# Kernel optimization log

Hardware: AMD Instinct MI355X
Metric: run time of the kernel (lower is better)

Reference implementation:

```python
import jax, jax.numpy as jnp
import numpy as np

B, T, C, H, N_LAYER, LAYER_ID = 4, 2048, 1024, 16, 12, 6
N = C // H
Q = 256  # T % 256 == 0 -> chunk size used by the module


def setup_inputs():
    key = jax.random.key(0)
    ks = jax.random.split(key, 9)
    r0 = LAYER_ID / (N_LAYER - 1)
    r1 = 1.0 - LAYER_ID / N_LAYER
    ddd = (jnp.arange(C, dtype=jnp.float32) / C)[None, None, :]
    h = jnp.arange(C, dtype=jnp.float32)
    s = 1.0 / np.sqrt(C)
    return {
        "x": jax.random.normal(ks[0], (B, T, C), jnp.float32),
        "time_maa_x": 1.0 - ddd ** r1,
        "time_maa_w": 1.0 - ddd ** r1,
        "time_maa_k": 1.0 - ddd ** r1,
        "time_maa_v": 1.0 - (ddd ** r1 + 0.3 * r0),
        "time_maa_r": 1.0 - ddd ** (0.5 * r1),
        "maa_w1": jax.random.uniform(ks[1], (C, 4 * 32), jnp.float32, minval=-0.01, maxval=0.01),
        "maa_w2": jax.random.uniform(ks[2], (4, 32, C), jnp.float32, minval=-0.01, maxval=0.01),
        "decay_w1": jax.random.uniform(ks[3], (C, 64), jnp.float32, minval=-0.01, maxval=0.01),
        "decay_w2": jax.random.uniform(ks[4], (64, C), jnp.float32, minval=-0.01, maxval=0.01),
        "time_decay": (-6.0 + 5.0 * (h / (C - 1)) ** (0.7 + 1.3 * r0))[None, None, :],
        "time_faaaa": (r0 * (1.0 - h / (C - 1))).reshape(1, H, 1, 1, N),
        "Wr": jax.random.normal(ks[5], (C, C), jnp.float32) * s,
        "Wk": jax.random.normal(ks[6], (C, C), jnp.float32) * s,
        "Wv": jax.random.normal(ks[7], (C, C), jnp.float32) * s,
        "Wo": jax.random.normal(ks[8], (C, C), jnp.float32) * s,
        "ln_g": jnp.ones((C,), jnp.float32),
        "ln_b": jnp.zeros((C,), jnp.float32),
    }


def _forward(x, time_maa_x, time_maa_w, time_maa_k, time_maa_v, time_maa_r,
             maa_w1, maa_w2, decay_w1, decay_w2, time_decay, time_faaaa,
             Wr, Wk, Wv, Wo, ln_g, ln_b):
    b, t, c = x.shape
    nc = t // Q
    # time_shift: zero-pad one step at front of time axis, drop last step
    xx = jnp.pad(x, ((0, 0), (1, 0), (0, 0)))[:, :-1] - x
    xxx = x + xx * time_maa_x
    m = jnp.tanh(xxx @ maa_w1).reshape(b, t, 4, -1)  # [B,T,4,32]
    m = jnp.einsum('btfd,fdc->fbtc', m, maa_w2)       # [4,B,T,C]
    mw, mk, mv, mr = m[0], m[1], m[2], m[3]
    xw = x + xx * (time_maa_w + mw)
    xk = x + xx * (time_maa_k + mk)
    xv = x + xx * (time_maa_v + mv)
    xr = x + xx * (time_maa_r + mr)
    r = (xr @ Wr).reshape(b, t, H, N).transpose(0, 2, 1, 3)  # [B,H,T,N]
    k = (xk @ Wk).reshape(b, t, H, N).transpose(0, 2, 1, 3)
    v = (xv @ Wv).reshape(b, t, H, N).transpose(0, 2, 1, 3)
    w = time_decay + jnp.tanh(xw @ decay_w1) @ decay_w2      # [B,T,C]
    w = w.reshape(b, t, H, N).transpose(0, 2, 1, 3).mean(axis=-1)  # [B,H,T]
    w_log = -jnp.exp(w)
    wc = w_log.reshape(b, H, nc, Q, 1)
    wc_cum = jnp.cumsum(wc, axis=-2)
    shifted = jnp.pad(wc_cum, ((0, 0), (0, 0), (0, 0), (1, 0), (0, 0)))[..., :-1, :]
    ws_log = wc.sum(axis=-2, keepdims=True)   # [B,H,nc,1,1]
    w_inter = jnp.exp(ws_log - wc_cum)        # [B,H,nc,Q,1]
    w_intra = jnp.exp(wc_cum - wc)            # [B,H,nc,Q,1]
    ws = jnp.exp(ws_log)                      # [B,H,nc,1,1]
    A = shifted - jnp.swapaxes(wc_cum, -1, -2)  # [B,H,nc,Q,Q]
    strict = jnp.tril(jnp.ones((Q, Q), dtype=bool), -1)
    # torch: tril() -> exp() -> tril(-1)  ==  exp on strict-lower, zero elsewhere
    w_mask = jnp.where(strict, jnp.exp(jnp.where(strict, A, 0.0)), 0.0)
    rr = r.reshape(b, H, nc, Q, N)
    kk = k.reshape(b, H, nc, Q, N)
    vv = v.reshape(b, H, nc, Q, N)
    kv = jnp.einsum('bhcqn,bhcqm->bhcnm', kk * w_inter, vv)  # [B,H,nc,N,N]

    def step(state, inp):
        ws_i, kv_i = inp
        return ws_i * state + kv_i, state  # emit state BEFORE update (as in torch loop)

    _, states = jax.lax.scan(step, jnp.zeros((b, H, N, N), x.dtype),
                             (jnp.moveaxis(ws, 2, 0), jnp.moveaxis(kv, 2, 0)))
    states = jnp.moveaxis(states, 0, 2)  # [B,H,nc,N,N]
    inter = jnp.einsum('bhcqn,bhcnm->bhcqm', rr * w_intra, states)
    scores = jnp.einsum('bhcqn,bhckn->bhcqk', rr, kk) * w_mask
    diag = jnp.sum(rr * (time_faaaa * kk), axis=-1)  # [B,H,nc,Q]
    intra = jnp.einsum('bhcqk,bhckm->bhcqm', scores, vv) + diag[..., None] * vv
    y = (inter + intra).reshape(b, H, t, N).transpose(0, 2, 1, 3).reshape(b, t, c)
    mu = y.mean(axis=-1, keepdims=True)
    var = ((y - mu) ** 2).mean(axis=-1, keepdims=True)
    y = (y - mu) / jnp.sqrt(var + 1e-5) * ln_g + ln_b  # ln_x
    return y @ Wo  # output projection (dropout p=0)


def reference(x, time_maa_x, time_maa_w, time_maa_k, time_maa_v, time_maa_r,
              maa_w1, maa_w2, decay_w1, decay_w2, time_decay, time_faaaa,
              Wr, Wk, Wv, Wo, ln_g, ln_b):
    return _forward(x, time_maa_x, time_maa_w, time_maa_k, time_maa_v, time_maa_r,
                    maa_w1, maa_w2, decay_w1, decay_w2, time_decay, time_faaaa,
                    Wr, Wk, Wv, Wo, ln_g, ln_b)
```

## Files before the change

### kernel.cpp

```cpp
#include <hip/hip_runtime.h>
#include <math.h>

#define BB 4
#define TT 2048
#define CC 1024
#define HH 16
#define NN 64
#define QQ 256
#define NCH 8
#define BT 8192

typedef unsigned short u16;
typedef __attribute__((ext_vector_type(8))) short bf16x8;
typedef __attribute__((ext_vector_type(4))) short bf16x4;
typedef __attribute__((ext_vector_type(4))) float f32x4;
typedef __attribute__((ext_vector_type(4))) u16 u16x4;

__device__ inline u16 f2b(float x) {
  union { float f; unsigned u; } v;
  v.f = x;
  unsigned r = v.u + 0x7FFFu + ((v.u >> 16) & 1u);
  return (u16)(r >> 16);
}
__device__ inline float b2f(u16 u) {
  union { unsigned u; float f; } v;
  v.u = ((unsigned)u) << 16;
  return v.f;
}
__device__ inline bf16x8 ldfrag(const u16* p) {
  bf16x4 lo = *(const bf16x4*)p;
  bf16x4 hi = *(const bf16x4*)(p + 4);
  return __builtin_shufflevector(lo, hi, 0, 1, 2, 3, 4, 5, 6, 7);
}
__device__ inline void stage_tile(const u16* __restrict__ g, size_t base,
                                  int pitch, int tid, u16* __restrict__ lds) {
#pragma unroll
  for (int it = 0; it < 2; it++) {
    int cidx = tid + it * 256;
    int r = cidx >> 3, c8 = (cidx & 7) * 8;
    bf16x8 v = *(const bf16x8*)(g + base + (size_t)r * pitch + c8);
    *(bf16x4*)(lds + r * 72 + c8) = __builtin_shufflevector(v, v, 0, 1, 2, 3);
    *(bf16x4*)(lds + r * 72 + c8 + 4) = __builtin_shufflevector(v, v, 4, 5, 6, 7);
  }
}

__global__ __launch_bounds__(256) void mix_kernel(const float* __restrict__ x,
                                                  const float* __restrict__ tmx,
                                                  float* __restrict__ xx,
                                                  u16* __restrict__ xxxb) {
  size_t e = ((size_t)blockIdx.x * 256 + threadIdx.x) * 4;
  int c = (int)(e & 1023);
  size_t row = e >> 10;
  int t = (int)(row & 2047);
  float4 xv = *(const float4*)(x + e);
  float4 pv = make_float4(0.f, 0.f, 0.f, 0.f);
  if (t > 0) pv = *(const float4*)(x + e - 1024);
  float4 d = make_float4(pv.x - xv.x, pv.y - xv.y, pv.z - xv.z, pv.w - xv.w);
  *(float4*)(xx + e) = d;
  u16x4 o;
  o.x = f2b(xv.x + d.x * tmx[c + 0]);
  o.y = f2b(xv.y + d.y * tmx[c + 1]);
  o.z = f2b(xv.z + d.z * tmx[c + 2]);
  o.w = f2b(xv.w + d.w * tmx[c + 3]);
  *(u16x4*)(xxxb + e) = o;
}

__global__ __launch_bounds__(256) void cvt_wT(const float* __restrict__ W0,
                                              const float* __restrict__ W1,
                                              const float* __restrict__ W2,
                                              const float* __restrict__ W3,
                                              u16* __restrict__ O0,
                                              u16* __restrict__ O1,
                                              u16* __restrict__ O2,
                                              u16* __restrict__ O3) {
  const float* W;
  u16* O;
  switch (blockIdx.z) {
    case 0: W = W0; O = O0; break;
    case 1: W = W1; O = O1; break;
    case 2: W = W2; O = O2; break;
    default: W = W3; O = O3; break;
  }
  __shared__ float t[64][65];
  int bx = blockIdx.x * 64;
  int by = blockIdx.y * 64;
#pragma unroll
  for (int it = 0; it < 16; it++) {
    int idx = it * 256 + threadIdx.x;
    int r = idx >> 6, c = idx & 63;
    t[r][c] = W[(size_t)(by + r) * 1024 + bx + c];
  }
  __syncthreads();
#pragma unroll
  for (int it = 0; it < 16; it++) {
    int idx = it * 256 + threadIdx.x;
    int n = idx >> 6, k = idx & 63;
    O[(size_t)(bx + n) * 1024 + by + k] = f2b(t[k][n]);
  }
}

__global__ __launch_bounds__(256) void cvt_T(const float* __restrict__ in,
                                             u16* __restrict__ out, int R, int C) {
  __shared__ float t[64][65];
  int c0 = blockIdx.x * 64, r0 = blockIdx.y * 64;
#pragma unroll
  for (int it = 0; it < 16; it++) {
    int idx = it * 256 + threadIdx.x;
    int r = idx >> 6, c = idx & 63;
    t[r][c] = in[(size_t)(r0 + r) * C + c0 + c];
  }
  __syncthreads();
#pragma unroll
  for (int it = 0; it < 16; it++) {
    int idx = it * 256 + threadIdx.x;
    int c = idx >> 6, r = idx & 63;
    out[(size_t)(c0 + c) * R + r0 + r] = f2b(t[r][c]);
  }
}

template <bool TANH>
__global__ __launch_bounds__(256) void gemm_bt_mfma(const u16* __restrict__ A,
                                                    const u16* __restrict__ Bt,
                                                    float* __restrict__ Cf,
                                                    u16* __restrict__ Cb,
                                                    int M, int N, int K) {
  __shared__ u16 As[128 * 32];
  __shared__ u16 Bs[128 * 32];
  const int tid = threadIdx.x;
  const int lane = tid & 63;
  const int row0 = blockIdx.y * 128;
  const int col0 = blockIdx.x * 128;
  const int wave = tid >> 6;
  const int wr = (wave >> 1) * 64;
  const int wc = (wave & 1) * 64;
  const int fr = lane & 15;
  const int fq = lane >> 4;

  f32x4 acc[4][4];
#pragma unroll
  for (int i = 0; i < 4; i++)
#pragma unroll
    for (int j = 0; j < 4; j++) acc[i][j] = (f32x4){0.f, 0.f, 0.f, 0.f};

  const int i0 = tid, i1 = tid + 256;
  const int ra0 = i0 >> 2, ca0 = (i0 & 3) * 8;
  const int ra1 = i1 >> 2, ca1 = (i1 & 3) * 8;

  for (int k0 = 0; k0 < K; k0 += 32) {
    __builtin_amdgcn_global_load_lds(
        (const __attribute__((address_space(1))) void*)(A + (size_t)(row0 + ra0) * K + k0 + ca0),
        (__attribute__((address_space(3))) void*)(As + i0 * 8), 16, 0, 0);
    __builtin_amdgcn_global_load_lds(
        (const __attribute__((address_space(1))) void*)(A + (size_t)(row0 + ra1) * K + k0 + ca1),
        (__attribute__((address_space(3))) void*)(As + i1 * 8), 16, 0, 0);
    __builtin_amdgcn_global_load_lds(
        (const __attribute__((address_space(1))) void*)(Bt + (size_t)(col0 + ra0) * K + k0 + ca0),
        (__attribute__((address_space(3))) void*)(Bs + i0 * 8), 16, 0, 0);
    __builtin_amdgcn_global_load_lds(
        (const __attribute__((address_space(1))) void*)(Bt + (size_t)(col0 + ra1) * K + k0 + ca1),
        (__attribute__((address_space(3))) void*)(Bs + i1 * 8), 16, 0, 0);
    __syncthreads();

    bf16x8 af[4], bf[4];
#pragma unroll
    for (int i = 0; i < 4; i++)
      af[i] = *(const bf16x8*)(As + ((wr + i * 16 + fr) * 32 + fq * 8));
#pragma unroll
    for (int j = 0; j < 4; j++)
      bf[j] = *(const bf16x8*)(Bs + ((wc + j * 16 + fr) * 32 + fq * 8));
#pragma unroll
    for (int i = 0; i < 4; i++)
#pragma unroll
      for (int j = 0; j < 4; j++)
        acc[i][j] = __builtin_amdgcn_mfma_f32_16x16x32_bf16(af[i], bf[j], acc[i][j], 0, 0, 0);
    __syncthreads();
  }
#pragma unroll
  for (int i = 0; i < 4; i++) {
    int grow = row0 + wr + i * 16 + fq * 4;
#pragma unroll
    for (int j = 0; j < 4; j++) {
      int gcol = col0 + wc + j * 16 + fr;
#pragma unroll
      for (int r = 0; r < 4; r++) {
        float vv = acc[i][j][r];
        if (TANH) vv = tanhf(vv);
        if (Cf) Cf[(size_t)(grow + r) * N + gcol] = vv;
        if (Cb) Cb[(size_t)(grow + r) * N + gcol] = f2b(vv);
      }
    }
  }
}

#define DP_ABUF 8192
#define DP_BBUF 16384
#define DP_SBUF 24576
#define DP_SMEM_BYTES 147456

template <bool TRIPLE, bool F32OUT>
__global__ __launch_bounds__(512, 2) void gemm_dp(
    const u16* __restrict__ A0, const u16* __restrict__ A1,
    const u16* __restrict__ A2, const u16* __restrict__ B0,
    const u16* __restrict__ B1, const u16* __restrict__ B2,
    float* __restrict__ Cf, u16* __restrict__ C0, u16* __restrict__ C1,
    u16* __restrict__ C2) {
  extern __shared__ __align__(16) u16 smem[];
  const int nwg = (int)(gridDim.x * gridDim.y * gridDim.z);
  const int wg = (int)(blockIdx.x + (blockIdx.y << 2) + (blockIdx.z << 8));
  const int cpx = nwg >> 3;
  const int swz = (wg & 7) * cpx + (wg >> 3);
  const int bx = swz & 3;
  const int by = (swz >> 2) & 63;
  const int bz = swz >> 8;

  const u16* __restrict__ A;
  const u16* __restrict__ Bt;
  u16* __restrict__ Cb;
  if (TRIPLE) {
    switch (bz) {
      case 0: A = A0; Bt = B0; Cb = C0; break;
      case 1: A = A1; Bt = B1; Cb = C1; break;
      default: A = A2; Bt = B2; Cb = C2; break;
    }
  } else {
    A = A0; Bt = B0; Cb = C0;
  }

  const int tid = threadIdx.x;
  const int lane = tid & 63;
  const int wave = tid >> 6;
  const int wr = (wave >> 2) * 64;
  const int wc = (wave & 3) * 64;
  const int fr = lane & 15;
  const int fq = lane >> 4;
  const int s8 = fr & 7;
  const int row0 = by * 128;
  const int col0 = bx * 256;

  int aoff[4][2], boff[4][2];
#pragma unroll
  for (int mi = 0; mi < 4; mi++)
#pragma unroll
    for (int ks = 0; ks < 2; ks++)
      aoff[mi][ks] = (wr + mi * 16 + fr) * 64 + (((ks * 4 + fq) ^ s8) * 8);
#pragma unroll
  for (int nj = 0; nj < 4; nj++)
#pragma unroll
    for (int ks = 0; ks < 2; ks++)
      boff[nj][ks] = (wc + nj * 16 + fr) * 64 + (((ks * 4 + fq) ^ s8) * 8);

  auto stage = [&](int kt, int q) {
    const u16* __restrict__ gA = A + (size_t)row0 * 1024 + kt * 64;
    const u16* __restrict__ gB = Bt + (size_t)col0 * 1024 + kt * 64;
    u16* dA = smem + q * DP_SBUF;
    u16* dB = dA + DP_ABUF;
#pragma unroll
    for (int p = 0; p < 2; p++) {
      int pos = tid + p * 512;
      int r = pos >> 3, gch = (pos & 7) ^ (r & 7);
      __builtin_amdgcn_global_load_lds(
          (const __attribute__((address_space(1))) void*)(gA + (size_t)r * 1024 + gch * 8),
          (__attribute__((address_space(3))) void*)(dA + pos * 8), 16, 0, 0);
    }
#pragma unroll
    for (int p = 0; p < 4; p++) {
      int pos = tid + p * 512;
      int r = pos >> 3, gch = (pos & 7) ^ (r & 7);
      __builtin_amdgcn_global_load_lds(
          (const __attribute__((address_space(1))) void*)(gB + (size_t)r * 1024 + gch * 8),
          (__attribute__((address_space(3))) void*)(dB + pos * 8), 16, 0, 0);
    }
  };

  f32x4 acc[4][4];
#pragma unroll
  for (int mi = 0; mi < 4; mi++)
#pragma unroll
    for (int nj = 0; nj < 4; nj++) acc[mi][nj] = (f32x4){0.f, 0.f, 0.f, 0.f};

  auto iter_body = [&](int qc, int qs, bool dostage, int t2) {
    if (dostage) stage(t2, qs);
    const u16* sA = smem + qc * DP_SBUF;
    const u16* sB = sA + DP_ABUF;
    bf16x8 av[4][2], bv[4][2];
#pragma unroll
    for (int mi = 0; mi < 4; mi++)
#pragma unroll
      for (int ks = 0; ks < 2; ks++)
        av[mi][ks] = *(const bf16x8*)(sA + aoff[mi][ks]);
#pragma unroll
    for (int nj = 0; nj < 4; nj++)
#pragma unroll
      for (int ks = 0; ks < 2; ks++)
        bv[nj][ks] = *(const bf16x8*)(sB + boff[nj][ks]);
    __builtin_amdgcn_s_setprio(1);
#pragma unroll
    for (int ks = 0; ks < 2; ks++)
#pragma unroll
      for (int mi = 0; mi < 4; mi++)
#pragma unroll
        for (int nj = 0; nj < 4; nj++)
          acc[mi][nj] = __builtin_amdgcn_mfma_f32_16x16x32_bf16(
              av[mi][ks], bv[nj][ks], acc[mi][nj], 0, 0, 0);
    __builtin_amdgcn_s_setprio(0);
  };

  stage(0, 0);
  stage(1, 1);
  int qc = 0, qs = 2;
  for (int t = 0; t < 14; t++) {
    asm volatile("s_waitcnt vmcnt(6)" ::: "memory");
    __builtin_amdgcn_s_barrier();
    iter_body(qc, qs, true, t + 2);
    qc = (qc == 2) ? 0 : qc + 1;
    qs = (qs == 2) ? 0 : qs + 1;
  }
  asm volatile("s_waitcnt vmcnt(6)" ::: "memory");
  __builtin_amdgcn_s_barrier();
  iter_body(qc, 0, false, 0);
  qc = (qc == 2) ? 0 : qc + 1;
  asm volatile("s_waitcnt vmcnt(0)" ::: "memory");
  __builtin_amdgcn_s_barrier();
  iter_body(qc, 0, false, 0);

#pragma unroll
  for (int mi = 0; mi < 4; mi++) {
    int grow = row0 + wr + mi * 16 + fq * 4;
#pragma unroll
    for (int nj = 0; nj < 4; nj++) {
      int gcol = col0 + wc + nj * 16 + fr;
#pragma unroll
      for (int r = 0; r < 4; r++) {
        if (F32OUT)
          Cf[(size_t)(grow + r) * 1024 + gcol] = acc[mi][nj][r];
        else
          Cb[(size_t)(grow + r) * 1024 + gcol] = f2b(acc[mi][nj][r]);
      }
    }
  }
}

__global__ __launch_bounds__(256) void blend_mfma(
    const u16* __restrict__ mb, const u16* __restrict__ w2T,
    const float* __restrict__ x, const float* __restrict__ xx,
    const float* __restrict__ tmw, const float* __restrict__ tmk,
    const float* __restrict__ tmv, const float* __restrict__ tmr,
    u16* __restrict__ xwb, u16* __restrict__ xkb, u16* __restrict__ xvb,
    u16* __restrict__ xrb) {
  __shared__ u16 mS[64 * 136];
  __shared__ u16 wS[64 * 136];
  const int tid = threadIdx.x;
  const int lane = tid & 63;
  const int w = tid >> 6;
  const int fr = lane & 15;
  const int fq = lane >> 4;
  const int c0 = blockIdx.x * 64;
  const int bt0 = blockIdx.y * 64;

#pragma unroll
  for (int it = 0; it < 4; it++) {
    int idx = tid + it * 256;
    int r = idx >> 4, c8 = (idx & 15) * 8;
    bf16x8 v = *(const bf16x8*)(mb + (size_t)(bt0 + r) * 128 + c8);
    *(bf16x4*)(mS + r * 136 + c8) = __builtin_shufflevector(v, v, 0, 1, 2, 3);
    *(bf16x4*)(mS + r * 136 + c8 + 4) = __builtin_shufflevector(v, v, 4, 5, 6, 7);
    bf16x8 u = *(const bf16x8*)(w2T + (size_t)(c0 + r) * 128 + c8);
    *(bf16x4*)(wS + r * 136 + c8) = __builtin_shufflevector(u, u, 0, 1, 2, 3);
    *(bf16x4*)(wS + r * 136 + c8 + 4) = __builtin_shufflevector(u, u, 4, 5, 6, 7);
  }
  __syncthreads();

  f32x4 acc[4][4];
#pragma unroll
  for (int j = 0; j < 4; j++)
#pragma unroll
    for (int f = 0; f < 4; f++) acc[j][f] = (f32x4){0.f, 0.f, 0.f, 0.f};

#pragma unroll
  for (int f = 0; f < 4; f++) {
    bf16x8 aA = ldfrag(mS + (w * 16 + fr) * 136 + f * 32 + fq * 8);
#pragma unroll
    for (int j = 0; j < 4; j++) {
      bf16x8 bB = ldfrag(wS + (j * 16 + fr) * 136 + f * 32 + fq * 8);
      acc[j][f] = __builtin_amdgcn_mfma_f32_16x16x32_bf16(aA, bB, acc[j][f], 0, 0, 0);
    }
  }

#pragma unroll
  for (int j = 0; j < 4; j++) {
    int c = c0 + j * 16 + fr;
    float w_ = tmw[c], k_ = tmk[c], v_ = tmv[c], r_ = tmr[c];
#pragma unroll
    for (int rr = 0; rr < 4; rr++) {
      int bt = bt0 + w * 16 + fq * 4 + rr;
      size_t g = (size_t)bt * 1024 + c;
      float xv_ = x[g], dx = xx[g];
      xwb[g] = f2b(xv_ + dx * (w_ + acc[j][0][rr]));
      xkb[g] = f2b(xv_ + dx * (k_ + acc[j][1][rr]));
      xvb[g] = f2b(xv_ + dx * (v_ + acc[j][2][rr]));
      xrb[g] = f2b(xv_ + dx * (r_ + acc[j][3][rr]));
    }
  }
}

__global__ __launch_bounds__(256) void dw2r_kernel(const float* __restrict__ dw2,
                                                   const float* __restrict__ td,
                                                   float* __restrict__ dw2r,
                                                   float* __restrict__ tdr,
                                                   u16* __restrict__ dw2rbT) {
  int idx = blockIdx.x * 256 + threadIdx.x;
  if (idx < 1024) {
    int j = idx >> 4, h = idx & 15;
    float s = 0.f;
    for (int n = 0; n < 64; n++) s += dw2[(size_t)j * 1024 + h * 64 + n];
    float m = s * (1.f / 64.f);
    dw2r[j * 16 + h] = m;
    dw2rbT[h * 64 + j] = f2b(m);
  }
  if (idx < 16) {
    float s = 0.f;
    for (int n = 0; n < 64; n++) s += td[idx * 64 + n];
    tdr[idx] = s * (1.f / 64.f);
  }
}

__global__ __launch_bounds__(256) void decay_mfma(const u16* __restrict__ xwb,
                                                  const u16* __restrict__ d1T,
                                                  const u16* __restrict__ dw2rbT,
                                                  const float* __restrict__ tdr,
                                                  float* __restrict__ wlog) {
  __shared__ u16 As[64 * 32];
  __shared__ u16 Bs[64 * 32];
  __shared__ u16 h1S[64 * 72];
  __shared__ u16 dwS[16 * 72];
  const int tid = threadIdx.x;
  const int lane = tid & 63;
  const int w = tid >> 6;
  const int fr = lane & 15;
  const int fq = lane >> 4;
  const int bt0 = blockIdx.x * 64;

#pragma unroll
  for (int it = 0; it < 4; it++) {
    int idx = tid + it * 256;
    int r = idx >> 6, c = idx & 63;
    dwS[r * 72 + c] = dw2rbT[r * 64 + c];
  }

  f32x4 acc[4];
#pragma unroll
  for (int j = 0; j < 4; j++) acc[j] = (f32x4){0.f, 0.f, 0.f, 0.f};

  const int ra = tid >> 2, ca = (tid & 3) * 8;
  for (int k0 = 0; k0 < 1024; k0 += 32) {
    __builtin_amdgcn_global_load_lds(
        (const __attribute__((address_space(1))) void*)(xwb + (size_t)(bt0 + ra) * 1024 + k0 + ca),
        (__attribute__((address_space(3))) void*)(As + tid * 8), 16, 0, 0);
    __builtin_amdgcn_global_load_lds(
        (const __attribute__((address_space(1))) void*)(d1T + (size_t)ra * 1024 + k0 + ca),
        (__attribute__((address_space(3))) void*)(Bs + tid * 8), 16, 0, 0);
    __syncthreads();
    bf16x8 aA = *(const bf16x8*)(As + ((w * 16 + fr) * 32 + fq * 8));
#pragma unroll
    for (int j = 0; j < 4; j++) {
      bf16x8 bB = *(const bf16x8*)(Bs + ((j * 16 + fr) * 32 + fq * 8));
      acc[j] = __builtin_amdgcn_mfma_f32_16x16x32_bf16(aA, bB, acc[j], 0, 0, 0);
    }
    __syncthreads();
  }
#pragma unroll
  for (int j = 0; j < 4; j++)
#pragma unroll
    for (int rr = 0; rr < 4; rr++)
      h1S[(w * 16 + fq * 4 + rr) * 72 + j * 16 + fr] = f2b(tanhf(acc[j][rr]));
  __syncthreads();

  f32x4 a2 = (f32x4){0.f, 0.f, 0.f, 0.f};
#pragma unroll
  for (int ks = 0; ks < 2; ks++) {
    bf16x8 aA = ldfrag(h1S + (w * 16 + fr) * 72 + ks * 32 + fq * 8);
    bf16x8 bB = ldfrag(dwS + fr * 72 + ks * 32 + fq * 8);
    a2 = __builtin_amdgcn_mfma_f32_16x16x32_bf16(aA, bB, a2, 0, 0, 0);
  }
  float tdv = tdr[fr];
#pragma unroll
  for (int rr = 0; rr < 4; rr++) {
    int bt = bt0 + w * 16 + fq * 4 + rr;
    int b = bt >> 11, tl = bt & 2047;
    wlog[((size_t)(b * 16 + fr)) * 2048 + tl] = -__expf(tdv + a2[rr]);
  }
}

__global__ __launch_bounds__(256) void wprep_kernel(const float* __restrict__ wlog,
                                                    float* __restrict__ cum,
                                                    float* __restrict__ excl,
                                                    float* __restrict__ wsl) {
  int bid = blockIdx.x;
  int c = bid & 7, bh = bid >> 3;
  int q = threadIdx.x;
  float v = wlog[(size_t)bh * 2048 + c * 256 + q];
  __shared__ float s[256];
  s[q] = v;
  float val = v;
  for (int off = 1; off < 256; off <<= 1) {
    __syncthreads();
    float t = (q >= off) ? s[q - off] : 0.f;
    __syncthreads();
    val += t;
    s[q] = val;
  }
  __syncthreads();
  float total = s[255];
  cum[(size_t)bid * 256 + q] = val;
  excl[(size_t)bid * 256 + q] = val - v;
  if (q == 0) wsl[bid] = total;
}

__global__ __launch_bounds__(256) void kvtrans2_kernel(
    const u16* __restrict__ vb, const u16* __restrict__ kb,
    const u16* __restrict__ rb, const float* __restrict__ faaaa,
    const float* __restrict__ cum, const float* __restrict__ wsl,
    u16* __restrict__ vT, u16* __restrict__ kTw, float* __restrict__ diagG) {
  int tt = blockIdx.x;
  int bh = blockIdx.y;
  int b = bh >> 4, h = bh & 15;
  int cc = tt >> 2;
  int bidc = bh * 8 + cc;
  __shared__ float tv[64][65];
  __shared__ float tk[64][65];
  __shared__ float wfac[64];
  __shared__ float faS[64];
  const int tid = threadIdx.x;
  float wslog = wsl[bidc];
  if (tid < 64) {
    wfac[tid] = __expf(wslog - cum[(size_t)bidc * 256 + (tt & 3) * 64 + tid]);
    faS[tid] = faaaa[h * 64 + tid];
  }
  __syncthreads();
  const int m = tid & 63;
  float fam = faS[m];
#pragma unroll
  for (int it = 0; it < 16; it++) {
    int r = it * 4 + (tid >> 6);
    size_t g = ((size_t)(b * TT + tt * 64 + r)) * CC + h * 64 + m;
    float vraw = b2f(vb[g]);
    float kraw = b2f(kb[g]);
    float rraw = b2f(rb[g]);
    tv[r][m] = vraw;
    tk[r][m] = kraw;
    float s = rraw * fam * kraw;
    s += __shfl_xor(s, 1);
    s += __shfl_xor(s, 2);
    s += __shfl_xor(s, 4);
    s += __shfl_xor(s, 8);
    s += __shfl_xor(s, 16);
    s += __shfl_xor(s, 32);
    if (m == 0) diagG[(size_t)bh * 2048 + tt * 64 + r] = s;
  }
  __syncthreads();
#pragma unroll
  for (int it = 0; it < 16; it++) {
    int idx = it * 256 + tid;
    int mm = idx >> 6, tl = idx & 63;
    size_t o = ((size_t)(bh * 64 + mm)) * TT + tt * 64 + tl;
    vT[o] = f2b(tv[tl][mm]);
    kTw[o] = f2b(tk[tl][mm] * wfac[tl]);
  }
}

__global__ __launch_bounds__(256) void kv_mfma(const u16* __restrict__ kTw,
                                               const u16* __restrict__ vT,
                                               float* __restrict__ kvb) {
  int bid = blockIdx.x;
  int c = bid & 7, bh = bid >> 3;
  __shared__ u16 kS[64 * 72];
  __shared__ u16 vS[64 * 72];
  const int tid = threadIdx.x;
  const int lane = tid & 63;
  const int w = tid >> 6;
  const int fr = lane & 15;
  const int fq = lane >> 4;
  f32x4 acc[4];
#pragma unroll
  for (int j = 0; j < 4; j++) acc[j] = (f32x4){0.f, 0.f, 0.f, 0.f};
  const size_t base = (size_t)bh * 64 * TT + c * QQ;
  for (int qt = 0; qt < 4; qt++) {
    __syncthreads();
    stage_tile(kTw, base + qt * 64, TT, tid, kS);
    stage_tile(vT, base + qt * 64, TT, tid, vS);
    __syncthreads();
#pragma unroll
    for (int ks = 0; ks < 2; ks++) {
      bf16x8 aA = ldfrag(kS + (w * 16 + fr) * 72 + ks * 32 + fq * 8);
#pragma unroll
      for (int j = 0; j < 4; j++) {
        bf16x8 bB = ldfrag(vS + (j * 16 + fr) * 72 + ks * 32 + fq * 8);
        acc[j] = __builtin_amdgcn_mfma_f32_16x16x32_bf16(aA, bB, acc[j], 0, 0, 0);
      }
    }
  }
#pragma unroll
  for (int j = 0; j < 4; j++)
#pragma unroll
    for (int rr = 0; rr < 4; rr++)
      kvb[(size_t)bid * 4096 + (w * 16 + fq * 4 + rr) * 64 + j * 16 + fr] = acc[j][rr];
}

__global__ __launch_bounds__(256) void scan_kernel(const float* __restrict__ kvb,
                                                   const float* __restrict__ wsl,
                                                   float* __restrict__ st) {
  int bh = blockIdx.x;
  int tid = threadIdx.x;
  float s[16];
#pragma unroll
  for (int i = 0; i < 16; i++) s[i] = 0.f;
  for (int c = 0; c < 8; c++) {
    int bid = bh * 8 + c;
    float w = __expf(wsl[bid]);
#pragma unroll
    for (int i = 0; i < 16; i++) {
      size_t e = (size_t)bid * 4096 + i * 256 + tid;
      st[e] = s[i];
      s[i] = w * s[i] + kvb[e];
    }
  }
}

__global__ __launch_bounds__(256) void attn_mfma(
    const u16* __restrict__ rb, const u16* __restrict__ kb,
    const u16* __restrict__ vT, const float* __restrict__ stg,
    const float* __restrict__ cum, const float* __restrict__ excl,
    const float* __restrict__ diagG, float* __restrict__ y) {
  int bid = blockIdx.x;
  int c = bid & 7, bh = bid >> 3;
  int b = bh >> 4, h = bh & 15;
  __shared__ u16 rt[64 * 72];
  __shared__ u16 kt[64 * 72];
  __shared__ u16 vt[64 * 72];
  __shared__ u16 pt[64 * 72];
  __shared__ u16 stT[64 * 72];
  __shared__ float cumS[256], exS[256], diagS[256], ekS[256];

  const int tid = threadIdx.x;
  const int lane = tid & 63;
  const int w = tid >> 6;
  const int fr = lane & 15;
  const int fq = lane >> 4;

  cumS[tid] = cum[(size_t)bid * 256 + tid];
  exS[tid] = excl[(size_t)bid * 256 + tid];
  diagS[tid] = diagG[(size_t)bh * 2048 + c * 256 + tid];
#pragma unroll
  for (int it = 0; it < 16; it++) {
    int idx = tid + it * 256;
    int n = idx >> 6, mm = idx & 63;
    stT[mm * 72 + n] = f2b(stg[(size_t)bid * 4096 + idx]);
  }
  __syncthreads();
  const float ccm = cumS[127];
  ekS[tid] = __expf(ccm - cumS[tid]);

  const size_t rowbase = ((size_t)b * TT + c * QQ) * CC + h * 64;
  const size_t vbase0 = (size_t)bh * 64 * TT + c * QQ;

  for (int qt = 0; qt < 4; qt++) {
    __syncthreads();
    stage_tile(rb, rowbase + (size_t)(qt * 64) * CC, CC, tid, rt);
    __syncthreads();

    f32x4 acc[4];
#pragma unroll
    for (int jm = 0; jm < 4; jm++) acc[jm] = (f32x4){0.f, 0.f, 0.f, 0.f};
    bf16x8 rA[2];
    rA[0] = ldfrag(rt + (w * 16 + fr) * 72 + fq * 8);
    rA[1] = ldfrag(rt + (w * 16 + fr) * 72 + 32 + fq * 8);
#pragma unroll
    for (int ks = 0; ks < 2; ks++)
#pragma unroll
      for (int jm = 0; jm < 4; jm++) {
        bf16x8 bB = ldfrag(stT + (jm * 16 + fr) * 72 + ks * 32 + fq * 8);
        acc[jm] = __builtin_amdgcn_mfma_f32_16x16x32_bf16(rA[ks], bB, acc[jm], 0, 0, 0);
      }
    int ql0 = w * 16 + fq * 4;
    float er[4], eqc[4];
#pragma unroll
    for (int rr = 0; rr < 4; rr++) {
      float ex = exS[qt * 64 + ql0 + rr];
      er[rr] = __expf(ex);
      eqc[rr] = __expf(ex - ccm);
    }
#pragma unroll
    for (int jm = 0; jm < 4; jm++)
#pragma unroll
      for (int rr = 0; rr < 4; rr++) acc[jm][rr] *= er[rr];

    for (int kti = 0; kti <= qt; kti++) {
      __syncthreads();
      stage_tile(kb, rowbase + (size_t)(kti * 64) * CC, CC, tid, kt);
      stage_tile(vT, vbase0 + (size_t)(kti * 64), TT, tid, vt);
      __syncthreads();

      f32x4 sacc[4];
#pragma unroll
      for (int jj = 0; jj < 4; jj++) sacc[jj] = (f32x4){0.f, 0.f, 0.f, 0.f};
#pragma unroll
      for (int ks = 0; ks < 2; ks++)
#pragma unroll
        for (int jj = 0; jj < 4; jj++) {
          bf16x8 bB = ldfrag(kt + (jj * 16 + fr) * 72 + ks * 32 + fq * 8);
          sacc[jj] = __builtin_amdgcn_mfma_f32_16x16x32_bf16(rA[ks], bB, sacc[jj], 0, 0, 0);
        }
#pragma unroll
      for (int jj = 0; jj < 4; jj++) {
        int kcol = kti * 64 + jj * 16 + fr;
        float ek = ekS[kcol];
#pragma unroll
        for (int rr = 0; rr < 4; rr++) {
          int qrow = qt * 64 + ql0 + rr;
          float vsc;
          if (kcol < qrow)
            vsc = sacc[jj][rr] * eqc[rr] * ek;
          else if (kcol == qrow)
            vsc = diagS[qrow];
          else
            vsc = 0.f;
          pt[(ql0 + rr) * 72 + jj * 16 + fr] = f2b(vsc);
        }
      }
      __syncthreads();
#pragma unroll
      for (int ks = 0; ks < 2; ks++) {
        bf16x8 pA = ldfrag(pt + (w * 16 + fr) * 72 + ks * 32 + fq * 8);
#pragma unroll
        for (int jm = 0; jm < 4; jm++) {
          bf16x8 vB = ldfrag(vt + (jm * 16 + fr) * 72 + ks * 32 + fq * 8);
          acc[jm] = __builtin_amdgcn_mfma_f32_16x16x32_bf16(pA, vB, acc[jm], 0, 0, 0);
        }
      }
    }
    int qg0 = qt * 64 + w * 16 + fq * 4;
#pragma unroll
    for (int jm = 0; jm < 4; jm++)
#pragma unroll
      for (int rr = 0; rr < 4; rr++)
        y[rowbase + (size_t)(qg0 + rr) * CC + jm * 16 + fr] = acc[jm][rr];
  }
}

__global__ __launch_bounds__(256) void ln_kernel(const float* __restrict__ y,
                                                 const float* __restrict__ g,
                                                 const float* __restrict__ bta,
                                                 u16* __restrict__ out) {
  __shared__ float red[8];
  int bt = blockIdx.x;
  int tid = threadIdx.x;
  float v[4];
  float s = 0.f;
#pragma unroll
  for (int i = 0; i < 4; i++) {
    v[i] = y[(size_t)bt * 1024 + i * 256 + tid];
    s += v[i];
  }
#pragma unroll
  for (int off = 32; off > 0; off >>= 1) s += __shfl_down(s, off);
  if ((tid & 63) == 0) red[tid >> 6] = s;
  __syncthreads();
  if (tid == 0) red[4] = red[0] + red[1] + red[2] + red[3];
  __syncthreads();
  float mu = red[4] * (1.f / 1024.f);
  float s2 = 0.f;
#pragma unroll
  for (int i = 0; i < 4; i++) {
    float d = v[i] - mu;
    s2 += d * d;
  }
#pragma unroll
  for (int off = 32; off > 0; off >>= 1) s2 += __shfl_down(s2, off);
  __syncthreads();
  if ((tid & 63) == 0) red[tid >> 6] = s2;
  __syncthreads();
  if (tid == 0) red[5] = red[0] + red[1] + red[2] + red[3];
  __syncthreads();
  float var = red[5] * (1.f / 1024.f);
  float rstd = rsqrtf(var + 1e-5f);
#pragma unroll
  for (int i = 0; i < 4; i++) {
    int c = i * 256 + tid;
    out[(size_t)bt * 1024 + c] = f2b((v[i] - mu) * rstd * g[c] + bta[c]);
  }
}

extern "C" void kernel_launch(void* const* d_in, const int* in_sizes, int n_in,
                              void* d_out, int out_size, void* d_ws,
                              size_t ws_size, hipStream_t stream) {
  const float* x = (const float*)d_in[0];
  const float* tmx = (const float*)d_in[1];
  const float* tmw = (const float*)d_in[2];
  const float* tmk = (const float*)d_in[3];
  const float* tmv = (const float*)d_in[4];
  const float* tmr = (const float*)d_in[5];
  const float* maa_w1 = (const float*)d_in[6];
  const float* maa_w2 = (const float*)d_in[7];
  const float* decay_w1 = (const float*)d_in[8];
  const float* decay_w2 = (const float*)d_in[9];
  const float* time_decay = (const float*)d_in[10];
  const float* faaaa = (const float*)d_in[11];
  const float* Wr = (const float*)d_in[12];
  const float* Wk = (const float*)d_in[13];
  const float* Wv = (const float*)d_in[14];
  const float* Wo = (const float*)d_in[15];
  const float* lng = (const float*)d_in[16];
  const float* lnb = (const float*)d_in[17];
  float* out = (float*)d_out;
  float* ws = (float*)d_ws;

  const size_t S = (size_t)BT * CC;

  float* xx = ws;
  float* dw2r = ws + S;
  float* tdr = dw2r + 1024;
  float* wlog = tdr + 1024;
  float* cum = wlog + 131072;
  float* excl = cum + 131072;
  float* wsl = excl + 131072;
  float* diagG = wsl + 1024;
  float* kvb = diagG + 131072;
  float* stb = kvb + (size_t)512 * 4096;
  float* fend = stb + (size_t)512 * 4096;
  u16* xxxb = (u16*)fend;
  u16* mb = xxxb + S;
  u16* xkb = mb + (size_t)BT * 128;
  u16* xvb = xkb + S;
  u16* xrb = xvb + S;
  u16* xwb = xrb + S;
  u16* rb16 = xwb + S;
  u16* kb16 = rb16 + S;
  u16* Vb = kb16 + S;
  u16* Wrt = Vb + S;
  u16* Wkt = Wrt + (size_t)1024 * 1024;
  u16* Wvt = Wkt + (size_t)1024 * 1024;
  u16* Wot = Wvt + (size_t)1024 * 1024;
  u16* w1T = Wot + (size_t)1024 * 1024;
  u16* w2T = w1T + (size_t)128 * 1024;
  u16* d1T = w2T + (size_t)1024 * 128;
  u16* dw2rbT = d1T + (size_t)64 * 1024;
  u16* vT = xxxb;
  u16* kTw = xrb;
  float* y_ = xx;
  u16* ylnb = xkb;

  static bool attr_done = false;
  if (!attr_done) {
    hipFuncSetAttribute((const void*)gemm_dp<true, false>,
                        hipFuncAttributeMaxDynamicSharedMemorySize, DP_SMEM_BYTES);
    hipFuncSetAttribute((const void*)gemm_dp<false, true>,
                        hipFuncAttributeMaxDynamicSharedMemorySize, DP_SMEM_BYTES);
    attr_done = true;
  }

  cvt_wT<<<dim3(16, 16, 4), 256, 0, stream>>>(Wr, Wk, Wv, Wo, Wrt, Wkt, Wvt, Wot);
  cvt_T<<<dim3(2, 16), 256, 0, stream>>>(maa_w1, w1T, 1024, 128);
  cvt_T<<<dim3(16, 2), 256, 0, stream>>>(maa_w2, w2T, 128, 1024);
  cvt_T<<<dim3(1, 16), 256, 0, stream>>>(decay_w1, d1T, 1024, 64);
  dw2r_kernel<<<4, 256, 0, stream>>>(decay_w2, time_decay, dw2r, tdr, dw2rbT);
  mix_kernel<<<8192, 256, 0, stream>>>(x, tmx, xx, xxxb);
  gemm_bt_mfma<true><<<dim3(1, 64), 256, 0, stream>>>(xxxb, w1T, nullptr, mb, BT, 128, CC);
  blend_mfma<<<dim3(16, 128), 256, 0, stream>>>(mb, w2T, x, xx, tmw, tmk, tmv,
                                                tmr, xwb, xkb, xvb, xrb);
  decay_mfma<<<128, 256, 0, stream>>>(xwb, d1T, dw2rbT, tdr, wlog);
  wprep_kernel<<<512, 256, 0, stream>>>(wlog, cum, excl, wsl);
  gemm_dp<true, false><<<dim3(4, 64, 3), 512, DP_SMEM_BYTES, stream>>>(
      xrb, xkb, xvb, Wrt, Wkt, Wvt, nullptr, rb16, kb16, Vb);
  kvtrans2_kernel<<<dim3(32, 64), 256, 0, stream>>>(Vb, kb16, rb16, faaaa, cum,
                                                    wsl, vT, kTw, diagG);
  kv_mfma<<<512, 256, 0, stream>>>(kTw, vT, kvb);
  scan_kernel<<<64, 256, 0, stream>>>(kvb, wsl, stb);
  attn_mfma<<<512, 256, 0, stream>>>(rb16, kb16, vT, stb, cum, excl, diagG, y_);
  ln_kernel<<<BT, 256, 0, stream>>>(y_, lng, lnb, ylnb);
  gemm_dp<false, true><<<dim3(4, 64, 1), 512, DP_SMEM_BYTES, stream>>>(
      ylnb, nullptr, nullptr, Wot, nullptr, nullptr, out, nullptr, nullptr,
      nullptr);
}
```

Measured before the change: 378.5 us.

## Drop xx buffer, merge weight transposes, retile maa GEMM, split scan blocks

Several independent changes. The time-shift difference is now recomputed in blend_mfma instead of being written as a full fp32 xx tensor by mix_kernel and read back, which removes a 32 MB round trip. The three small weight-transpose launches are merged into one, and the maa GEMM uses 64-row tiles so it launches 128 blocks instead of 64. The scan kernel is split four ways per head to use 256 blocks instead of 64. The cost is an extra read of the previous row of x in blend and some early-exit blocks in the merged transpose.

```diff
diff --git a/kernel.cpp b/kernel.cpp
--- a/kernel.cpp
+++ b/kernel.cpp
@@ -46,7 +46,6 @@
 
 __global__ __launch_bounds__(256) void mix_kernel(const float* __restrict__ x,
                                                   const float* __restrict__ tmx,
-                                                  float* __restrict__ xx,
                                                   u16* __restrict__ xxxb) {
   size_t e = ((size_t)blockIdx.x * 256 + threadIdx.x) * 4;
   int c = (int)(e & 1023);
@@ -56,7 +55,6 @@
   float4 pv = make_float4(0.f, 0.f, 0.f, 0.f);
   if (t > 0) pv = *(const float4*)(x + e - 1024);
   float4 d = make_float4(pv.x - xv.x, pv.y - xv.y, pv.z - xv.z, pv.w - xv.w);
-  *(float4*)(xx + e) = d;
   u16x4 o;
   o.x = f2b(xv.x + d.x * tmx[c + 0]);
   o.y = f2b(xv.y + d.y * tmx[c + 1]);
@@ -99,10 +97,23 @@
   }
 }
 
-__global__ __launch_bounds__(256) void cvt_T(const float* __restrict__ in,
-                                             u16* __restrict__ out, int R, int C) {
+__global__ __launch_bounds__(256) void cvt3_T(const float* __restrict__ w1,
+                                              const float* __restrict__ w2,
+                                              const float* __restrict__ d1,
+                                              u16* __restrict__ o1,
+                                              u16* __restrict__ o2,
+                                              u16* __restrict__ o3) {
+  const float* in;
+  u16* out;
+  int R, C;
+  switch (blockIdx.z) {
+    case 0: in = w1; out = o1; R = 1024; C = 128; break;
+    case 1: in = w2; out = o2; R = 128; C = 1024; break;
+    default: in = d1; out = o3; R = 1024; C = 64; break;
+  }
+  int c0 = blockIdx.x * 64, r0 = blockIdx.y * 64;
+  if (c0 >= C || r0 >= R) return;
   __shared__ float t[64][65];
-  int c0 = blockIdx.x * 64, r0 = blockIdx.y * 64;
 #pragma unroll
   for (int it = 0; it < 16; it++) {
     int idx = it * 256 + threadIdx.x;
@@ -118,76 +129,62 @@
   }
 }
 
-template <bool TANH>
-__global__ __launch_bounds__(256) void gemm_bt_mfma(const u16* __restrict__ A,
-                                                    const u16* __restrict__ Bt,
-                                                    float* __restrict__ Cf,
-                                                    u16* __restrict__ Cb,
-                                                    int M, int N, int K) {
-  __shared__ u16 As[128 * 32];
+__global__ __launch_bounds__(256) void gemm_maa(const u16* __restrict__ A,
+                                                const u16* __restrict__ Bt,
+                                                u16* __restrict__ Cb) {
+  __shared__ u16 As[64 * 32];
   __shared__ u16 Bs[128 * 32];
   const int tid = threadIdx.x;
   const int lane = tid & 63;
-  const int row0 = blockIdx.y * 128;
-  const int col0 = blockIdx.x * 128;
   const int wave = tid >> 6;
-  const int wr = (wave >> 1) * 64;
-  const int wc = (wave & 1) * 64;
+  const int wc = wave * 32;
   const int fr = lane & 15;
   const int fq = lane >> 4;
-
-  f32x4 acc[4][4];
+  const int row0 = blockIdx.x * 64;
+
+  f32x4 acc[4][2];
 #pragma unroll
   for (int i = 0; i < 4; i++)
 #pragma unroll
-    for (int j = 0; j < 4; j++) acc[i][j] = (f32x4){0.f, 0.f, 0.f, 0.f};
-
-  const int i0 = tid, i1 = tid + 256;
-  const int ra0 = i0 >> 2, ca0 = (i0 & 3) * 8;
-  const int ra1 = i1 >> 2, ca1 = (i1 & 3) * 8;
-
-  for (int k0 = 0; k0 < K; k0 += 32) {
+    for (int j = 0; j < 2; j++) acc[i][j] = (f32x4){0.f, 0.f, 0.f, 0.f};
+
+  const int ra = tid >> 2, ca = (tid & 3) * 8;
+  const int rb1 = ra + 64;
+
+  for (int k0 = 0; k0 < 1024; k0 += 32) {
     __builtin_amdgcn_global_load_lds(
-        (const __attribute__((address_space(1))) void*)(A + (size_t)(row0 + ra0) * K + k0 + ca0),
-        (__attribute__((address_space(3))) void*)(As + i0 * 8), 16, 0, 0);
+        (const __attribute__((address_space(1))) void*)(A + (size_t)(row0 + ra) * 1024 + k0 + ca),
+        (__attribute__((address_space(3))) void*)(As + tid * 8), 16, 0, 0);
     __builtin_amdgcn_global_load_lds(
-        (const __attribute__((address_space(1))) void*)(A + (size_t)(row0 + ra1) * K + k0 + ca1),
-        (__attribute__((address_space(3))) void*)(As + i1 * 8), 16, 0, 0);
+        (const __attribute__((address_space(1))) void*)(Bt + (size_t)ra * 1024 + k0 + ca),
+        (__attribute__((address_space(3))) void*)(Bs + tid * 8), 16, 0, 0);
     __builtin_amdgcn_global_load_lds(
-        (const __attribute__((address_space(1))) void*)(Bt + (size_t)(col0 + ra0) * K + k0 + ca0),
-        (__attribute__((address_space(3))) void*)(Bs + i0 * 8), 16, 0, 0);
-    __builtin_amdgcn_global_load_lds(
-        (const __attribute__((address_space(1))) void*)(Bt + (size_t)(col0 + ra1) * K + k0 + ca1),
-        (__attribute__((address_space(3))) void*)(Bs + i1 * 8), 16, 0, 0);
-    __syncthreads();
-
-    bf16x8 af[4], bf[4];
+        (const __attribute__((address_space(1))) void*)(Bt + (size_t)rb1 * 1024 + k0 + ca),
+        (__attribute__((address_space(3))) void*)(Bs + (tid + 256) * 8), 16, 0, 0);
+    __syncthreads();
+    bf16x8 af[4], bf[2];
 #pragma unroll
     for (int i = 0; i < 4; i++)
-      af[i] = *(const bf16x8*)(As + ((wr + i * 16 + fr) * 32 + fq * 8));
-#pragma unroll
-    for (int j = 0; j < 4; j++)
+      af[i] = *(const bf16x8*)(As + ((i * 16 + fr) * 32 + fq * 8));
+#pragma unroll
+    for (int j = 0; j < 2; j++)
       bf[j] = *(const bf16x8*)(Bs + ((wc + j * 16 + fr) * 32 + fq * 8));
 #pragma unroll
     for (int i = 0; i < 4; i++)
 #pragma unroll
-      for (int j = 0; j < 4; j++)
+      for (int j = 0; j < 2; j++)
         acc[i][j] = __builtin_amdgcn_mfma_f32_16x16x32_bf16(af[i], bf[j], acc[i][j], 0, 0, 0);
     __syncthreads();
   }
 #pragma unroll
   for (int i = 0; i < 4; i++) {
-    int grow = row0 + wr + i * 16 + fq * 4;
-#pragma unroll
-    for (int j = 0; j < 4; j++) {
-      int gcol = col0 + wc + j * 16 + fr;
-#pragma unroll
-      for (int r = 0; r < 4; r++) {
-        float vv = acc[i][j][r];
-        if (TANH) vv = tanhf(vv);
-        if (Cf) Cf[(size_t)(grow + r) * N + gcol] = vv;
-        if (Cb) Cb[(size_t)(grow + r) * N + gcol] = f2b(vv);
-      }
+    int grow = row0 + i * 16 + fq * 4;
+#pragma unroll
+    for (int j = 0; j < 2; j++) {
+      int gcol = wc + j * 16 + fr;
+#pragma unroll
+      for (int r = 0; r < 4; r++)
+        Cb[(size_t)(grow + r) * 128 + gcol] = f2b(tanhf(acc[i][j][r]));
     }
   }
 }
@@ -342,7 +339,7 @@
 
 __global__ __launch_bounds__(256) void blend_mfma(
     const u16* __restrict__ mb, const u16* __restrict__ w2T,
-    const float* __restrict__ x, const float* __restrict__ xx,
+    const float* __restrict__ x,
     const float* __restrict__ tmw, const float* __restrict__ tmk,
     const float* __restrict__ tmv, const float* __restrict__ tmr,
     u16* __restrict__ xwb, u16* __restrict__ xkb, u16* __restrict__ xvb,
@@ -394,7 +391,9 @@
     for (int rr = 0; rr < 4; rr++) {
       int bt = bt0 + w * 16 + fq * 4 + rr;
       size_t g = (size_t)bt * 1024 + c;
-      float xv_ = x[g], dx = xx[g];
+      float xv_ = x[g];
+      float xp = ((bt & 2047) != 0) ? x[g - 1024] : 0.f;
+      float dx = xp - xv_;
       xwb[g] = f2b(xv_ + dx * (w_ + acc[j][0][rr]));
       xkb[g] = f2b(xv_ + dx * (k_ + acc[j][1][rr]));
       xvb[g] = f2b(xv_ + dx * (v_ + acc[j][2][rr]));
@@ -609,17 +608,18 @@
 __global__ __launch_bounds__(256) void scan_kernel(const float* __restrict__ kvb,
                                                    const float* __restrict__ wsl,
                                                    float* __restrict__ st) {
-  int bh = blockIdx.x;
+  int bh = blockIdx.x >> 2;
+  int sl = blockIdx.x & 3;
   int tid = threadIdx.x;
-  float s[16];
-#pragma unroll
-  for (int i = 0; i < 16; i++) s[i] = 0.f;
+  float s[4];
+#pragma unroll
+  for (int i = 0; i < 4; i++) s[i] = 0.f;
   for (int c = 0; c < 8; c++) {
     int bid = bh * 8 + c;
     float w = __expf(wsl[bid]);
 #pragma unroll
-    for (int i = 0; i < 16; i++) {
-      size_t e = (size_t)bid * 4096 + i * 256 + tid;
+    for (int i = 0; i < 4; i++) {
+      size_t e = (size_t)bid * 4096 + sl * 1024 + i * 256 + tid;
       st[e] = s[i];
       s[i] = w * s[i] + kvb[e];
     }
@@ -816,7 +816,7 @@
 
   const size_t S = (size_t)BT * CC;
 
-  float* xx = ws;
+  float* y_ = ws;
   float* dw2r = ws + S;
   float* tdr = dw2r + 1024;
   float* wlog = tdr + 1024;
@@ -846,7 +846,6 @@
   u16* dw2rbT = d1T + (size_t)64 * 1024;
   u16* vT = xxxb;
   u16* kTw = xrb;
-  float* y_ = xx;
   u16* ylnb = xkb;
 
   static bool attr_done = false;
@@ -859,14 +858,13 @@
   }
 
   cvt_wT<<<dim3(16, 16, 4), 256, 0, stream>>>(Wr, Wk, Wv, Wo, Wrt, Wkt, Wvt, Wot);
-  cvt_T<<<dim3(2, 16), 256, 0, stream>>>(maa_w1, w1T, 1024, 128);
-  cvt_T<<<dim3(16, 2), 256, 0, stream>>>(maa_w2, w2T, 128, 1024);
-  cvt_T<<<dim3(1, 16), 256, 0, stream>>>(decay_w1, d1T, 1024, 64);
+  cvt3_T<<<dim3(16, 16, 3), 256, 0, stream>>>(maa_w1, maa_w2, decay_w1, w1T,
+                                              w2T, d1T);
   dw2r_kernel<<<4, 256, 0, stream>>>(decay_w2, time_decay, dw2r, tdr, dw2rbT);
-  mix_kernel<<<8192, 256, 0, stream>>>(x, tmx, xx, xxxb);
-  gemm_bt_mfma<true><<<dim3(1, 64), 256, 0, stream>>>(xxxb, w1T, nullptr, mb, BT, 128, CC);
-  blend_mfma<<<dim3(16, 128), 256, 0, stream>>>(mb, w2T, x, xx, tmw, tmk, tmv,
-                                                tmr, xwb, xkb, xvb, xrb);
+  mix_kernel<<<8192, 256, 0, stream>>>(x, tmx, xxxb);
+  gemm_maa<<<128, 256, 0, stream>>>(xxxb, w1T, mb);
+  blend_mfma<<<dim3(16, 128), 256, 0, stream>>>(mb, w2T, x, tmw, tmk, tmv, tmr,
+                                                xwb, xkb, xvb, xrb);
   decay_mfma<<<128, 256, 0, stream>>>(xwb, d1T, dw2rbT, tdr, wlog);
   wprep_kernel<<<512, 256, 0, stream>>>(wlog, cum, excl, wsl);
   gemm_dp<true, false><<<dim3(4, 64, 3), 512, DP_SMEM_BYTES, stream>>>(
@@ -874,7 +872,7 @@
   kvtrans2_kernel<<<dim3(32, 64), 256, 0, stream>>>(Vb, kb16, rb16, faaaa, cum,
                                                     wsl, vT, kTw, diagG);
   kv_mfma<<<512, 256, 0, stream>>>(kTw, vT, kvb);
-  scan_kernel<<<64, 256, 0, stream>>>(kvb, wsl, stb);
+  scan_kernel<<<256, 256, 0, stream>>>(kvb, wsl, stb);
   attn_mfma<<<512, 256, 0, stream>>>(rb16, kb16, vT, stb, cum, excl, diagG, y_);
   ln_kernel<<<BT, 256, 0, stream>>>(y_, lng, lnb, ylnb);
   gemm_dp<false, true><<<dim3(4, 64, 1), 512, DP_SMEM_BYTES, stream>>>(
```

After: 365.0 us. 3.6% less time.
